# Optimization experiments

Measured on AMD Instinct MI355X. Metric: run time of the kernel, lower is better.

The kernel has to match this reference:

```python
import jax, jax.numpy as jnp
import numpy as np

B, S, HID = 2, 2048, 2048
NH, NKV, D = 32, 8, 64
G = NH // NKV
THETA = 150000.0


def rotate_half(x):
    x1, x2 = x[..., : D // 2], x[..., D // 2 :]
    return jnp.concatenate([-x2, x1], axis=-1)


def setup_inputs() -> dict:
    key = jax.random.key(0)
    ks = jax.random.split(key, 10)
    sc = 0.02
    return {
        "hidden_states": jax.random.normal(ks[0], (B, S, HID), jnp.float32),
        "position_ids": jnp.arange(S, dtype=jnp.int64 if jax.config.jax_enable_x64 else jnp.int32),
        "wq": jax.random.normal(ks[1], (HID, NH * D), jnp.float32) * sc,
        "bq": jax.random.normal(ks[2], (NH * D,), jnp.float32) * sc,
        "wk": jax.random.normal(ks[3], (HID, NKV * D), jnp.float32) * sc,
        "bk": jax.random.normal(ks[4], (NKV * D,), jnp.float32) * sc,
        "wv": jax.random.normal(ks[5], (HID, NKV * D), jnp.float32) * sc,
        "bv": jax.random.normal(ks[6], (NKV * D,), jnp.float32) * sc,
        "wo": jax.random.normal(ks[7], (NH * D, HID), jnp.float32) * sc,
        "bo": jax.random.normal(ks[8], (HID,), jnp.float32) * sc,
    }


def reference(hidden_states, position_ids, wq, bq, wk, bk, wv, bv, wo, bo):
    # projections: [B,S,NH,D] / [B,S,NKV,D] -> head-major
    q = (hidden_states @ wq + bq).reshape(B, S, NH, D).transpose(0, 2, 1, 3)   # [B,NH,S,D]
    k = (hidden_states @ wk + bk).reshape(B, S, NKV, D).transpose(0, 2, 1, 3)  # [B,NKV,S,D]
    v = (hidden_states @ wv + bv).reshape(B, S, NKV, D).transpose(0, 2, 1, 3)

    # HF RoPE: inv_freq over even dims, freqs duplicated across the two halves
    inv_freq = 1.0 / (THETA ** (jnp.arange(0, D, 2, dtype=jnp.float32) / D))   # [D/2]
    freqs = position_ids.astype(jnp.float32)[:, None] * inv_freq[None, :]      # [S,D/2]
    emb = jnp.concatenate([freqs, freqs], axis=-1)                             # [S,D]
    cos = jnp.cos(emb)[None, None]  # [1,1,S,D]
    sin = jnp.sin(emb)[None, None]
    q = q * cos + rotate_half(q) * sin
    k = k * cos + rotate_half(k) * sin

    # GQA: group query heads by kv head instead of repeat_interleave on K/V
    qg = q.reshape(B, NKV, G, S, D)
    scores = jnp.einsum("bkgsd,bktd->bkgst", qg, k) / jnp.sqrt(jnp.float32(D))  # [B,NKV,G,S,S]
    attn = jax.nn.softmax(scores, axis=-1)
    out = jnp.einsum("bkgst,bktd->bkgsd", attn, v)                              # [B,NKV,G,S,D]
    out = out.reshape(B, NH, S, D).transpose(0, 2, 1, 3).reshape(B, S, NH * D)  # [B,S,NH*D]
    return out @ wo + bo
```

## Files before the change

kernel.cpp:

```cpp
#include <hip/hip_runtime.h>
#include <hip/hip_bf16.h>
#include <math.h>

#define B_   2
#define S_   2048
#define HID_ 2048
#define NH_  32
#define NKV_ 8
#define D_   64
#define G_   (NH_/NKV_)
#define M_   (B_*S_)

typedef __hip_bfloat16 bf16;
typedef short bf16x8 __attribute__((ext_vector_type(8)));
typedef float f32x4  __attribute__((ext_vector_type(4)));
typedef unsigned short u16x4 __attribute__((ext_vector_type(4)));

__device__ inline unsigned short f2bfu(float f){
    __hip_bfloat16 h = __float2bfloat16(f);
    return __builtin_bit_cast(unsigned short, h);
}

__device__ __forceinline__ float fexp2(float x){
#if __has_builtin(__builtin_amdgcn_exp2f)
    return __builtin_amdgcn_exp2f(x);
#else
    return exp2f(x);
#endif
}

__device__ __forceinline__ void async16(const void* g, void* l) {
    __builtin_amdgcn_global_load_lds(
        (const __attribute__((address_space(1))) unsigned int*)g,
        (__attribute__((address_space(3))) unsigned int*)l, 16, 0, 0);
}

#define SWZ(r, c) ((c) ^ (((r) & 7) << 3))

#define S_BARRIER() asm volatile("s_barrier" ::: "memory")
__device__ __forceinline__ void vmwait8(){ asm volatile("s_waitcnt vmcnt(8)" ::: "memory"); }
__device__ __forceinline__ void vmwait6(){ asm volatile("s_waitcnt vmcnt(6)" ::: "memory"); }
__device__ __forceinline__ void vmwait0(){ asm volatile("s_waitcnt vmcnt(0)" ::: "memory"); }

__global__ __launch_bounds__(256) void cvt_k(
    const float* __restrict__ src, bf16* __restrict__ dst, int n)
{
    const int i = (blockIdx.x * 256 + threadIdx.x) * 8;
    if (i >= n) return;
    const float4 a = *(const float4*)(src + i);
    const float4 b = *(const float4*)(src + i + 4);
    uint4 u;
    u.x = (unsigned)f2bfu(a.x) | ((unsigned)f2bfu(a.y) << 16);
    u.y = (unsigned)f2bfu(a.z) | ((unsigned)f2bfu(a.w) << 16);
    u.z = (unsigned)f2bfu(b.x) | ((unsigned)f2bfu(b.y) << 16);
    u.w = (unsigned)f2bfu(b.z) | ((unsigned)f2bfu(b.w) << 16);
    *(uint4*)((unsigned short*)dst + i) = u;
}

__global__ __launch_bounds__(256) void wtrans_k(
    const float* __restrict__ s0, int N0,
    const float* __restrict__ s1, int N1,
    const float* __restrict__ s2, int N2,
    bf16* __restrict__ dst, int K)
{
    __shared__ unsigned short t[64][65];
    const int ntile = blockIdx.x * 64, ktile = blockIdx.y * 64;
    const float* src; int nloc, Nseg;
    if (ntile < N0)           { src = s0; nloc = ntile;           Nseg = N0; }
    else if (ntile < N0 + N1) { src = s1; nloc = ntile - N0;      Nseg = N1; }
    else                      { src = s2; nloc = ntile - N0 - N1; Nseg = N2; }
    const int r  = threadIdx.x >> 4;
    const int c4 = (threadIdx.x & 15) * 4;
    #pragma unroll
    for (int p = 0; p < 4; p++) {
        const int k = p * 16 + r;
        const float4 f = *(const float4*)(src + (size_t)(ktile + k) * Nseg + nloc + c4);
        t[k][c4+0] = f2bfu(f.x); t[k][c4+1] = f2bfu(f.y);
        t[k][c4+2] = f2bfu(f.z); t[k][c4+3] = f2bfu(f.w);
    }
    __syncthreads();
    #pragma unroll
    for (int p = 0; p < 4; p++) {
        const int n = p * 16 + r;
        u16x4 u = { t[c4+0][n], t[c4+1][n], t[c4+2][n], t[c4+3][n] };
        *(u16x4*)((unsigned short*)dst + (size_t)(ntile + n) * K + ktile + c4) = u;
    }
}

__global__ __launch_bounds__(256) void rope_tab_k(
    const int* __restrict__ pos, float* __restrict__ ctab, float* __restrict__ stab)
{
    const int idx = blockIdx.x * 256 + threadIdx.x;
    if (idx >= S_ * 32) return;
    const int s = idx >> 5, i = idx & 31;
    const int is64 = (pos[1] == 0);
    const int p = is64 ? pos[2 * s] : pos[s];
    const double inv = exp(-(double)i * (log(150000.0) / 32.0));
    const double f = (double)p * inv;
    ctab[idx] = (float)cos(f);
    stab[idx] = (float)sin(f);
}


template<int BM>
__device__ __forceinline__ void stage_g(
    const bf16* __restrict__ A, const bf16* __restrict__ B,
    int m0, int n0, int k0,
    unsigned short* sAb, unsigned short* sBb, int wave, int lane)
{
    const int rr = wave * 8 + (lane >> 3);
    const int cc = ((lane & 7) ^ (lane >> 3)) * 8;
    #pragma unroll
    for (int i = 0; i < BM / 64; ++i)
        async16(A + (size_t)(m0 + i * 64 + rr) * 2048 + k0 + cc,
                sAb + i * 4096 + wave * 512);
    #pragma unroll
    for (int j = 0; j < 4; ++j)
        async16(B + (size_t)(n0 + j * 64 + rr) * 2048 + k0 + cc,
                sBb + j * 4096 + wave * 512);
}

template<int BM>
__device__ __forceinline__ void tile_mfma(
    const unsigned short* sAb, const unsigned short* sBb,
    int wm, int wn, int li, int lj, f32x4 (*acc)[4])
{
    constexpr int MT = BM / 32;
    constexpr int PM = MT / 4;
    const int swz = li & 7;

    bf16x8 bfr[4][2];
    #pragma unroll
    for (int nt = 0; nt < 4; ++nt)
        #pragma unroll
        for (int ks = 0; ks < 2; ++ks)
            bfr[nt][ks] = *(const bf16x8*)
                &sBb[(wn * 64 + nt * 16 + li) * 64 + ((ks * 4 + lj) ^ swz) * 8];

    bf16x8 afA[PM][2], afB[PM][2];
    auto lda = [&](bf16x8 (*dst)[2], int p) {
        #pragma unroll
        for (int m = 0; m < PM; ++m)
            #pragma unroll
            for (int ks = 0; ks < 2; ++ks)
                dst[m][ks] = *(const bf16x8*)
                    &sAb[(wm * (BM / 2) + (p * PM + m) * 16 + li) * 64
                         + ((ks * 4 + lj) ^ swz) * 8];
    };
    lda(afA, 0);
    #pragma unroll
    for (int p = 0; p < 4; ++p) {
        bf16x8 (*cur)[2] = (p & 1) ? afB : afA;
        bf16x8 (*nxt)[2] = (p & 1) ? afA : afB;
        if (p < 3) lda(nxt, p + 1);
        __builtin_amdgcn_s_setprio(1);
        #pragma unroll
        for (int ks = 0; ks < 2; ++ks)
            #pragma unroll
            for (int m = 0; m < PM; ++m)
                #pragma unroll
                for (int nt = 0; nt < 4; ++nt)
                    acc[p * PM + m][nt] = __builtin_amdgcn_mfma_f32_16x16x32_bf16(
                        cur[m][ks], bfr[nt][ks], acc[p * PM + m][nt], 0, 0, 0);
        __builtin_amdgcn_s_setprio(0);
        __builtin_amdgcn_sched_barrier(0);
    }
}

template<int MODE, int BM>
__global__ __launch_bounds__(512, 2) void gemm256_k(
    const bf16* __restrict__ A, const bf16* __restrict__ WT,
    const float* __restrict__ b0, const float* __restrict__ b1,
    const float* __restrict__ b2,
    bf16* __restrict__ Cq, bf16* __restrict__ Ck, bf16* __restrict__ Cv,
    float* __restrict__ Cout,
    const float* __restrict__ ctab, const float* __restrict__ stab)
{
    constexpr int MT = BM / 32;
    constexpr int LA = BM * 64;
    constexpr int LB = 256 * 64;
    constexpr int NT = 2048 / 64;
    __shared__ unsigned short sA[2 * LA];
    __shared__ unsigned short sB[2 * LB];

    const int tid  = threadIdx.x;
    const int wave = tid >> 6, lane = tid & 63;
    const int li   = lane & 15, lj = lane >> 4;
    const int wm   = wave >> 2, wn = wave & 3;
    const int m0   = blockIdx.y * BM;
    const int n0   = blockIdx.x * 256;

    f32x4 acc[MT][4];
    #pragma unroll
    for (int i = 0; i < MT; ++i)
        #pragma unroll
        for (int j = 0; j < 4; ++j)
            acc[i][j] = (f32x4){0.f, 0.f, 0.f, 0.f};

    stage_g<BM>(A, WT, m0, n0, 0,  sA,      sB,      wave, lane);
    stage_g<BM>(A, WT, m0, n0, 64, sA + LA, sB + LB, wave, lane);
    if constexpr (BM == 256) vmwait8(); else vmwait6();
    S_BARRIER();

    for (int t = 0; t < NT; ++t) {
        const int buf = t & 1;
        tile_mfma<BM>(sA + buf * LA, sB + buf * LB, wm, wn, li, lj, acc);
        S_BARRIER();
        if (t + 2 < NT) {
            stage_g<BM>(A, WT, m0, n0, (t + 2) * 64,
                        sA + buf * LA, sB + buf * LB, wave, lane);
            if constexpr (BM == 256) vmwait8(); else vmwait6();
        } else {
            vmwait0();
        }
        S_BARRIER();
    }

    if (MODE == 1) {
        #pragma unroll
        for (int mt = 0; mt < MT; ++mt)
            #pragma unroll
            for (int nt = 0; nt < 4; ++nt) {
                const int col = n0 + wn * 64 + nt * 16 + li;
                const float bb = b0[col];
                #pragma unroll
                for (int r = 0; r < 4; ++r) {
                    const int row = m0 + wm * (BM / 2) + mt * 16 + lj * 4 + r;
                    Cout[(size_t)row * HID_ + col] = acc[mt][nt][r] + bb;
                }
            }
        return;
    }

    int seg, cb; const float* bias;
    if (n0 < 2048)      { seg = 0; cb = n0;        bias = b0; }
    else if (n0 < 2560) { seg = 1; cb = n0 - 2048; bias = b1; }
    else                { seg = 2; cb = n0 - 2560; bias = b2; }

    float bl[4];
    #pragma unroll
    for (int nt = 0; nt < 4; ++nt) bl[nt] = bias[cb + wn * 64 + nt * 16 + li];

    if (seg == 2) {
        const int b = m0 >> 11;
        #pragma unroll
        for (int nt = 0; nt < 4; ++nt) {
            const int cseg = cb + wn * 64 + nt * 16 + li;
            const int hv = cseg >> 6, d = cseg & 63;
            #pragma unroll
            for (int mt = 0; mt < MT; ++mt) {
                const int sb = (m0 & (S_ - 1)) + wm * (BM / 2) + mt * 16 + lj * 4;
                u16x4 u = { f2bfu(acc[mt][nt][0] + bl[nt]),
                            f2bfu(acc[mt][nt][1] + bl[nt]),
                            f2bfu(acc[mt][nt][2] + bl[nt]),
                            f2bfu(acc[mt][nt][3] + bl[nt]) };
                *(u16x4*)((unsigned short*)Cv +
                    ((size_t)((b * NKV_ + hv) * 64 + d)) * S_ + sb) = u;
            }
        }
        return;
    }

    const float qs = (seg == 0) ? 0.18033688011112042f : 1.0f;
    #pragma unroll
    for (int mt = 0; mt < MT; ++mt) {
        #pragma unroll
        for (int r = 0; r < 4; ++r) {
            const int row = m0 + wm * (BM / 2) + mt * 16 + lj * 4 + r;
            const int s = row & (S_ - 1);
            const float c0  = ctab[s * 32 + li],      sn0 = stab[s * 32 + li];
            const float c1  = ctab[s * 32 + 16 + li], sn1 = stab[s * 32 + 16 + li];
            const float x0 = acc[mt][0][r] + bl[0];
            const float x1 = acc[mt][1][r] + bl[1];
            const float x2 = acc[mt][2][r] + bl[2];
            const float x3 = acc[mt][3][r] + bl[3];
            const float y0 = (x0 * c0 - x2 * sn0) * qs;
            const float y2 = (x2 * c0 + x0 * sn0) * qs;
            const float y1 = (x1 * c1 - x3 * sn1) * qs;
            const float y3 = (x3 * c1 + x1 * sn1) * qs;
            if (seg == 0) {
                bf16* cp = Cq + (size_t)row * HID_ + n0 + wn * 64 + li;
                cp[0]  = __float2bfloat16(y0);
                cp[16] = __float2bfloat16(y1);
                cp[32] = __float2bfloat16(y2);
                cp[48] = __float2bfloat16(y3);
            } else {
                bf16* cp = Ck + (size_t)row * 512 + cb + wn * 64 + li;
                cp[0]  = __float2bfloat16(y0);
                cp[16] = __float2bfloat16(y1);
                cp[32] = __float2bfloat16(y2);
                cp[48] = __float2bfloat16(y3);
            }
        }
    }
}

__global__ __launch_bounds__(256, 4) void attn_k(
    const bf16* __restrict__ qws, const bf16* __restrict__ kws,
    const bf16* __restrict__ vtw, bf16* __restrict__ ows)
{
    __shared__ unsigned short sK [64 * 64];
    __shared__ unsigned short sVt[64 * 64];
    __shared__ unsigned short sP [4 * 32 * 64];

    const int tid  = threadIdx.x;
    const int wave = tid >> 6, lane = tid & 63;
    const int li   = lane & 15, lj = lane >> 4;
    const int bh   = blockIdx.y;
    const int q0   = blockIdx.x * 128;
    const int b    = bh / NH_, h = bh % NH_;
    const int hk   = h / G_;

    bf16x8 qf[2][2];
    #pragma unroll
    for (int g = 0; g < 2; g++) {
        const bf16* qp = qws + (size_t)(b * S_ + q0 + wave * 32 + g * 16 + li) * HID_
                         + h * D_ + lj * 8;
        qf[g][0] = *(const bf16x8*)(qp);
        qf[g][1] = *(const bf16x8*)(qp + 32);
    }

    f32x4 o[2][4];
    #pragma unroll
    for (int g = 0; g < 2; g++)
        #pragma unroll
        for (int mt = 0; mt < 4; mt++) o[g][mt] = (f32x4){0.f, 0.f, 0.f, 0.f};
    float mr[2] = {-1e30f, -1e30f};
    float ll[2] = {0.f, 0.f};

    const int srow = tid >> 2, scol = (tid & 3) * 16;
    const bf16* kb = kws + (size_t)b * S_ * 512 + hk * 64;
    const bf16* vb = vtw + (size_t)((b * NKV_ + hk) * 64) * S_;
    unsigned short* sp = sP + wave * (32 * 64);

    uint4 pk0, pk1, pv0, pv1;
    {
        const uint4* kp = (const uint4*)(kb + (size_t)srow * 512 + scol);
        const uint4* vp = (const uint4*)(vb + (size_t)srow * S_ + scol);
        pk0 = kp[0]; pk1 = kp[1]; pv0 = vp[0]; pv1 = vp[1];
    }

    for (int kt = 0; kt < S_; kt += 64) {
        __syncthreads();
        *(uint4*)&sK [srow * 64 + SWZ(srow, scol)]     = pk0;
        *(uint4*)&sK [srow * 64 + SWZ(srow, scol + 8)] = pk1;
        *(uint4*)&sVt[srow * 64 + SWZ(srow, scol)]     = pv0;
        *(uint4*)&sVt[srow * 64 + SWZ(srow, scol + 8)] = pv1;
        __syncthreads();

        if (kt + 64 < S_) {
            const uint4* kp = (const uint4*)(kb + (size_t)(kt + 64 + srow) * 512 + scol);
            const uint4* vp = (const uint4*)(vb + (size_t)srow * S_ + kt + 64 + scol);
            pk0 = kp[0]; pk1 = kp[1]; pv0 = vp[0]; pv1 = vp[1];
        }

        float sc[2][4][4];
        __builtin_amdgcn_s_setprio(1);
        #pragma unroll
        for (int nt = 0; nt < 4; nt++) {
            f32x4 c0 = (f32x4){0.f, 0.f, 0.f, 0.f};
            f32x4 c1 = (f32x4){0.f, 0.f, 0.f, 0.f};
            #pragma unroll
            for (int ks = 0; ks < 2; ks++) {
                const bf16x8 kf =
                    *(const bf16x8*)&sK[(nt * 16 + li) * 64 + SWZ(li, ks * 32 + lj * 8)];
                c0 = __builtin_amdgcn_mfma_f32_16x16x32_bf16(kf, qf[0][ks], c0, 0, 0, 0);
                c1 = __builtin_amdgcn_mfma_f32_16x16x32_bf16(kf, qf[1][ks], c1, 0, 0, 0);
            }
            #pragma unroll
            for (int r = 0; r < 4; r++) { sc[0][nt][r] = c0[r]; sc[1][nt][r] = c1[r]; }
        }
        __builtin_amdgcn_s_setprio(0);

        #pragma unroll
        for (int g = 0; g < 2; g++) {
            float cm = sc[g][0][0];
            #pragma unroll
            for (int nt = 0; nt < 4; nt++)
                #pragma unroll
                for (int r = 0; r < 4; r++) cm = fmaxf(cm, sc[g][nt][r]);
            cm = fmaxf(cm, __shfl_xor(cm, 16));
            cm = fmaxf(cm, __shfl_xor(cm, 32));
            if (!__all(cm - mr[g] <= 8.0f)) {
                const float mnew = fmaxf(mr[g], cm);
                const float al   = fexp2(mr[g] - mnew);
                mr[g] = mnew;
                ll[g] *= al;
                #pragma unroll
                for (int mt = 0; mt < 4; mt++) o[g][mt] *= al;
            }
            float rs = 0.f;
            #pragma unroll
            for (int nt = 0; nt < 4; nt++) {
                const float e0 = fexp2(sc[g][nt][0] - mr[g]);
                const float e1 = fexp2(sc[g][nt][1] - mr[g]);
                const float e2 = fexp2(sc[g][nt][2] - mr[g]);
                const float e3 = fexp2(sc[g][nt][3] - mr[g]);
                rs += (e0 + e1) + (e2 + e3);
                u16x4 u = { f2bfu(e0), f2bfu(e1), f2bfu(e2), f2bfu(e3) };
                *(u16x4*)&sp[(g * 16 + li) * 64 + SWZ(li, nt * 16 + lj * 4)] = u;
            }
            ll[g] += rs;
        }

        __builtin_amdgcn_s_setprio(1);
        #pragma unroll
        for (int ks = 0; ks < 2; ks++) {
            const bf16x8 pf0 = *(const bf16x8*)&sp[(li)      * 64 + SWZ(li, ks * 32 + lj * 8)];
            const bf16x8 pf1 = *(const bf16x8*)&sp[(16 + li) * 64 + SWZ(li, ks * 32 + lj * 8)];
            #pragma unroll
            for (int mt = 0; mt < 4; mt++) {
                const bf16x8 vf =
                    *(const bf16x8*)&sVt[(mt * 16 + li) * 64 + SWZ(li, ks * 32 + lj * 8)];
                o[0][mt] = __builtin_amdgcn_mfma_f32_16x16x32_bf16(vf, pf0, o[0][mt], 0, 0, 0);
                o[1][mt] = __builtin_amdgcn_mfma_f32_16x16x32_bf16(vf, pf1, o[1][mt], 0, 0, 0);
            }
        }
        __builtin_amdgcn_s_setprio(0);
    }

    #pragma unroll
    for (int g = 0; g < 2; g++) {
        float l = ll[g];
        l += __shfl_xor(l, 16);
        l += __shfl_xor(l, 32);
        const float inv = 1.0f / l;
        bf16* op = ows + (size_t)(b * S_ + q0 + wave * 32 + g * 16 + li) * HID_ + h * D_;
        #pragma unroll
        for (int mt = 0; mt < 4; mt++) {
            u16x4 u = { f2bfu(o[g][mt][0] * inv), f2bfu(o[g][mt][1] * inv),
                        f2bfu(o[g][mt][2] * inv), f2bfu(o[g][mt][3] * inv) };
            *(u16x4*)((unsigned short*)op + mt * 16 + lj * 4) = u;
        }
    }
}

extern "C" void kernel_launch(void* const* d_in, const int* in_sizes, int n_in,
                              void* d_out, int out_size, void* d_ws, size_t ws_size,
                              hipStream_t stream)
{
    const float* hs  = (const float*)d_in[0];
    const int*   pos = (const int*)d_in[1];
    const float* wq = (const float*)d_in[2];
    const float* bq = (const float*)d_in[3];
    const float* wk = (const float*)d_in[4];
    const float* bk = (const float*)d_in[5];
    const float* wv = (const float*)d_in[6];
    const float* bv = (const float*)d_in[7];
    const float* wo = (const float*)d_in[8];
    const float* bo = (const float*)d_in[9];

    char* ws = (char*)d_ws;
    float* ctab  = (float*)(ws);
    float* stab  = (float*)(ws + (256u << 10));
    bf16*  k_ws  = (bf16*)(ws + (512u << 10));
    bf16*  v_t   = (bf16*)(ws + (512u << 10) + (4u  << 20));
    bf16*  q_ws  = (bf16*)(ws + (512u << 10) + (8u  << 20));
    bf16*  woT   = q_ws;
    bf16*  hs_b  = (bf16*)(ws + (512u << 10) + (24u << 20));
    bf16*  o_ws  = hs_b;
    bf16*  wqkvT = (bf16*)(ws + (512u << 10) + (40u << 20));

    rope_tab_k<<<dim3(256), dim3(256), 0, stream>>>(pos, ctab, stab);

    cvt_k<<<dim3(M_ * HID_ / 2048), dim3(256), 0, stream>>>(hs, hs_b, M_ * HID_);

    wtrans_k<<<dim3(48, 32), dim3(256), 0, stream>>>(
        wq, 2048, wk, 512, wv, 512, wqkvT, HID_);

    gemm256_k<0, 256><<<dim3(12, 16), dim3(512), 0, stream>>>(
        hs_b, wqkvT, bq, bk, bv, q_ws, k_ws, v_t, nullptr, ctab, stab);

    attn_k<<<dim3(S_ / 128, B_ * NH_), dim3(256), 0, stream>>>(q_ws, k_ws, v_t, o_ws);

    wtrans_k<<<dim3(32, 32), dim3(256), 0, stream>>>(
        wo, 2048, wo, 0, wo, 0, woT, HID_);

    gemm256_k<1, 128><<<dim3(8, 32), dim3(512), 0, stream>>>(
        o_ws, woT, bo, nullptr, nullptr, nullptr, nullptr, nullptr,
        (float*)d_out, nullptr, nullptr);
}
```

Measured before the change: 347.4 us.

## Restructure GEMM main loop into eight-phase interleaved load/MFMA schedule

Replaces the double-buffered GEMM loop, which staged a whole A+B tile and then ran all MFMAs, with a finer schedule. Each K-tile is split into four quarter phases. Global-to-LDS async loads for the next A and B slabs are spread across these phases and separated by barriers, so memory traffic overlaps MFMA work more evenly. B fragments are loaded into registers once per tile, which frees the B buffer for refill earlier. The cost is many more s_barriers per iteration, plus redundant wrapped loads in the final iteration, which add sync overhead and wasted bandwidth.

```diff
diff --git a/kernel.cpp b/kernel.cpp
--- a/kernel.cpp
+++ b/kernel.cpp
@@ -38,8 +38,7 @@
 #define SWZ(r, c) ((c) ^ (((r) & 7) << 3))
 
 #define S_BARRIER() asm volatile("s_barrier" ::: "memory")
-__device__ __forceinline__ void vmwait8(){ asm volatile("s_waitcnt vmcnt(8)" ::: "memory"); }
-__device__ __forceinline__ void vmwait6(){ asm volatile("s_waitcnt vmcnt(6)" ::: "memory"); }
+__device__ __forceinline__ void vmwait4(){ asm volatile("s_waitcnt vmcnt(4)" ::: "memory"); }
 __device__ __forceinline__ void vmwait0(){ asm volatile("s_waitcnt vmcnt(0)" ::: "memory"); }
 
 __global__ __launch_bounds__(256) void cvt_k(
@@ -102,73 +101,17 @@
 }
 
 
-template<int BM>
-__device__ __forceinline__ void stage_g(
-    const bf16* __restrict__ A, const bf16* __restrict__ B,
-    int m0, int n0, int k0,
-    unsigned short* sAb, unsigned short* sBb, int wave, int lane)
+__device__ __forceinline__ void slab64(
+    const bf16* __restrict__ g, int grow0, int k0,
+    unsigned short* lds, int wave, int lane)
 {
     const int rr = wave * 8 + (lane >> 3);
     const int cc = ((lane & 7) ^ (lane >> 3)) * 8;
-    #pragma unroll
-    for (int i = 0; i < BM / 64; ++i)
-        async16(A + (size_t)(m0 + i * 64 + rr) * 2048 + k0 + cc,
-                sAb + i * 4096 + wave * 512);
-    #pragma unroll
-    for (int j = 0; j < 4; ++j)
-        async16(B + (size_t)(n0 + j * 64 + rr) * 2048 + k0 + cc,
-                sBb + j * 4096 + wave * 512);
-}
-
-template<int BM>
-__device__ __forceinline__ void tile_mfma(
-    const unsigned short* sAb, const unsigned short* sBb,
-    int wm, int wn, int li, int lj, f32x4 (*acc)[4])
-{
-    constexpr int MT = BM / 32;
-    constexpr int PM = MT / 4;
-    const int swz = li & 7;
-
-    bf16x8 bfr[4][2];
-    #pragma unroll
-    for (int nt = 0; nt < 4; ++nt)
-        #pragma unroll
-        for (int ks = 0; ks < 2; ++ks)
-            bfr[nt][ks] = *(const bf16x8*)
-                &sBb[(wn * 64 + nt * 16 + li) * 64 + ((ks * 4 + lj) ^ swz) * 8];
-
-    bf16x8 afA[PM][2], afB[PM][2];
-    auto lda = [&](bf16x8 (*dst)[2], int p) {
-        #pragma unroll
-        for (int m = 0; m < PM; ++m)
-            #pragma unroll
-            for (int ks = 0; ks < 2; ++ks)
-                dst[m][ks] = *(const bf16x8*)
-                    &sAb[(wm * (BM / 2) + (p * PM + m) * 16 + li) * 64
-                         + ((ks * 4 + lj) ^ swz) * 8];
-    };
-    lda(afA, 0);
-    #pragma unroll
-    for (int p = 0; p < 4; ++p) {
-        bf16x8 (*cur)[2] = (p & 1) ? afB : afA;
-        bf16x8 (*nxt)[2] = (p & 1) ? afA : afB;
-        if (p < 3) lda(nxt, p + 1);
-        __builtin_amdgcn_s_setprio(1);
-        #pragma unroll
-        for (int ks = 0; ks < 2; ++ks)
-            #pragma unroll
-            for (int m = 0; m < PM; ++m)
-                #pragma unroll
-                for (int nt = 0; nt < 4; ++nt)
-                    acc[p * PM + m][nt] = __builtin_amdgcn_mfma_f32_16x16x32_bf16(
-                        cur[m][ks], bfr[nt][ks], acc[p * PM + m][nt], 0, 0, 0);
-        __builtin_amdgcn_s_setprio(0);
-        __builtin_amdgcn_sched_barrier(0);
-    }
+    async16(g + (size_t)(grow0 + rr) * 2048 + k0 + cc, lds + wave * 512);
 }
 
 template<int MODE, int BM>
-__global__ __launch_bounds__(512, 2) void gemm256_k(
+__global__ __launch_bounds__(512, 2) void gemm8p_k(
     const bf16* __restrict__ A, const bf16* __restrict__ WT,
     const float* __restrict__ b0, const float* __restrict__ b1,
     const float* __restrict__ b2,
@@ -177,9 +120,10 @@
     const float* __restrict__ ctab, const float* __restrict__ stab)
 {
     constexpr int MT = BM / 32;
+    constexpr int PM = MT / 4;
     constexpr int LA = BM * 64;
     constexpr int LB = 256 * 64;
-    constexpr int NT = 2048 / 64;
+    constexpr int NT = 32;
     __shared__ unsigned short sA[2 * LA];
     __shared__ unsigned short sB[2 * LB];
 
@@ -189,6 +133,7 @@
     const int wm   = wave >> 2, wn = wave & 3;
     const int m0   = blockIdx.y * BM;
     const int n0   = blockIdx.x * 256;
+    const int swz  = li & 7;
 
     f32x4 acc[MT][4];
     #pragma unroll
@@ -197,24 +142,93 @@
         for (int j = 0; j < 4; ++j)
             acc[i][j] = (f32x4){0.f, 0.f, 0.f, 0.f};
 
-    stage_g<BM>(A, WT, m0, n0, 0,  sA,      sB,      wave, lane);
-    stage_g<BM>(A, WT, m0, n0, 64, sA + LA, sB + LB, wave, lane);
-    if constexpr (BM == 256) vmwait8(); else vmwait6();
+    bf16x8 bfr[4][2];
+
+    auto stageA = [&](int t, int r0) {
+        unsigned short* l = sA + (t & 1) * LA + r0 * 64;
+        const int k0 = (t & (NT - 1)) * 64;
+        slab64(A, m0 + r0,      k0, l,            wave, lane);
+        slab64(A, m0 + r0 + 64, k0, l + 64 * 64,  wave, lane);
+    };
+    auto stageB = [&](int t, int r0) {
+        unsigned short* l = sB + (t & 1) * LB + r0 * 64;
+        const int k0 = (t & (NT - 1)) * 64;
+        slab64(WT, n0 + r0,      k0, l,           wave, lane);
+        slab64(WT, n0 + r0 + 64, k0, l + 64 * 64, wave, lane);
+    };
+    auto ldB = [&](int tb) {
+        const unsigned short* base = sB + tb * LB;
+        #pragma unroll
+        for (int nt = 0; nt < 4; ++nt)
+            #pragma unroll
+            for (int ks = 0; ks < 2; ++ks)
+                bfr[nt][ks] = *(const bf16x8*)
+                    &base[(wn * 64 + nt * 16 + li) * 64 + ((ks * 4 + lj) ^ swz) * 8];
+    };
+    auto ldA = [&](int tb, int q, bf16x8 (*af)[2]) {
+        const unsigned short* base = sA + tb * LA;
+        #pragma unroll
+        for (int m = 0; m < PM; ++m)
+            #pragma unroll
+            for (int ks = 0; ks < 2; ++ks)
+                af[m][ks] = *(const bf16x8*)
+                    &base[(wm * (BM / 2) + (q * PM + m) * 16 + li) * 64
+                          + ((ks * 4 + lj) ^ swz) * 8];
+    };
+    auto mfma_q = [&](int q, bf16x8 (*af)[2]) {
+        __builtin_amdgcn_s_setprio(1);
+        #pragma unroll
+        for (int ks = 0; ks < 2; ++ks)
+            #pragma unroll
+            for (int m = 0; m < PM; ++m)
+                #pragma unroll
+                for (int nt = 0; nt < 4; ++nt)
+                    acc[q * PM + m][nt] = __builtin_amdgcn_mfma_f32_16x16x32_bf16(
+                        af[m][ks], bfr[nt][ks], acc[q * PM + m][nt], 0, 0, 0);
+        __builtin_amdgcn_s_setprio(0);
+    };
+
+    stageA(0, 0);
+    if constexpr (BM == 256) stageA(0, 128);
+    stageB(0, 0); stageB(0, 128);
+    stageB(1, 0); stageB(1, 128);
+    vmwait4();
     S_BARRIER();
 
-    for (int t = 0; t < NT; ++t) {
-        const int buf = t & 1;
-        tile_mfma<BM>(sA + buf * LA, sB + buf * LB, wm, wn, li, lj, acc);
+    for (int i = 0; i < NT / 2; ++i) {
+        const int ta = 2 * i, tb = 2 * i + 1;
+        bf16x8 af0[PM][2], af1[PM][2], af2[PM][2], af3[PM][2];
+        ldB(0); ldA(0, 0, af0);
+        stageA(tb, 0);
+        S_BARRIER(); mfma_q(0, af0); S_BARRIER();
+        ldA(0, 1, af1);
+        if constexpr (BM == 256) stageA(tb, 128);
+        S_BARRIER(); mfma_q(1, af1); S_BARRIER();
+        ldA(0, 2, af2);
+        stageB(ta + 2, 0);
+        S_BARRIER(); mfma_q(2, af2); S_BARRIER();
+        ldA(0, 3, af3);
+        stageB(ta + 2, 128);
+        S_BARRIER(); mfma_q(3, af3);
+        vmwait4();
         S_BARRIER();
-        if (t + 2 < NT) {
-            stage_g<BM>(A, WT, m0, n0, (t + 2) * 64,
-                        sA + buf * LA, sB + buf * LB, wave, lane);
-            if constexpr (BM == 256) vmwait8(); else vmwait6();
-        } else {
-            vmwait0();
-        }
+        ldB(1); ldA(1, 0, af0);
+        stageA(ta + 2, 0);
+        S_BARRIER(); mfma_q(0, af0); S_BARRIER();
+        ldA(1, 1, af1);
+        if constexpr (BM == 256) stageA(ta + 2, 128);
+        S_BARRIER(); mfma_q(1, af1); S_BARRIER();
+        ldA(1, 2, af2);
+        stageB(tb + 2, 0);
+        S_BARRIER(); mfma_q(2, af2); S_BARRIER();
+        ldA(1, 3, af3);
+        stageB(tb + 2, 128);
+        S_BARRIER(); mfma_q(3, af3);
+        vmwait4();
         S_BARRIER();
     }
+    vmwait0();
+    S_BARRIER();
 
     if (MODE == 1) {
         #pragma unroll
@@ -468,7 +482,7 @@
     wtrans_k<<<dim3(48, 32), dim3(256), 0, stream>>>(
         wq, 2048, wk, 512, wv, 512, wqkvT, HID_);
 
-    gemm256_k<0, 256><<<dim3(12, 16), dim3(512), 0, stream>>>(
+    gemm8p_k<0, 256><<<dim3(12, 16), dim3(512), 0, stream>>>(
         hs_b, wqkvT, bq, bk, bv, q_ws, k_ws, v_t, nullptr, ctab, stab);
 
     attn_k<<<dim3(S_ / 128, B_ * NH_), dim3(256), 0, stream>>>(q_ws, k_ws, v_t, o_ws);
@@ -476,7 +490,7 @@
     wtrans_k<<<dim3(32, 32), dim3(256), 0, stream>>>(
         wo, 2048, wo, 0, wo, 0, woT, HID_);
 
-    gemm256_k<1, 128><<<dim3(8, 32), dim3(512), 0, stream>>>(
+    gemm8p_k<1, 128><<<dim3(8, 32), dim3(512), 0, stream>>>(
         o_ws, woT, bo, nullptr, nullptr, nullptr, nullptr, nullptr,
         (float*)d_out, nullptr, nullptr);
 }
```

New measurement: 338.0 us. 2.7% less time.
